# Kernel optimization log

Measured on AMD Instinct MI355X. Metric: run time of the kernel, lower is better.

## Reference

```python
import jax, jax.numpy as jnp
import numpy as np

HIDDEN = 1024
NHEAD = 16
HEAD_DIM = HIDDEN // NHEAD
B, S = 2, 2048


def setup_inputs() -> dict:
    key = jax.random.key(0)
    ks = jax.random.split(key, 10)
    scale = 1.0 / np.sqrt(HIDDEN)
    inp = {
        "x": jax.random.normal(ks[0], (B, S, HIDDEN), dtype=jnp.float32),
        "mask": jax.random.randint(ks[1], (B, S), 0, 2).astype(bool),
        "Wq": jax.random.normal(ks[2], (HIDDEN, HIDDEN), dtype=jnp.float32) * scale,
        "bq": jnp.zeros((HIDDEN,), dtype=jnp.float32),
        "Wk": jax.random.normal(ks[3], (HIDDEN, HIDDEN), dtype=jnp.float32) * scale,
        "bk": jnp.zeros((HIDDEN,), dtype=jnp.float32),
        "Wv": jax.random.normal(ks[4], (HIDDEN, HIDDEN), dtype=jnp.float32) * scale,
        "bv": jnp.zeros((HIDDEN,), dtype=jnp.float32),
        "Wo": jax.random.normal(ks[5], (HIDDEN, HIDDEN), dtype=jnp.float32) * scale,
        "bo": jnp.zeros((HIDDEN,), dtype=jnp.float32),
    }
    return inp


def reference(x, mask, Wq, bq, Wk, bk, Wv, bv, Wo, bo):
    B_, S_, H = x.shape
    # QKV projections (torch Linear: x @ W.T + b), split into heads -> [B, nhead, S, head_dim]
    def split_heads(t):
        return t.reshape(B_, S_, NHEAD, HEAD_DIM).transpose(0, 2, 1, 3)

    q = split_heads(x @ Wq.T + bq)
    k = split_heads(x @ Wk.T + bk)
    v = split_heads(x @ Wv.T + bv)

    # scaled dot-product scores: [B, nhead, S, S]
    energy = jnp.einsum("bhqd,bhkd->bhqk", q, k) / jnp.sqrt(jnp.float32(HEAD_DIM))

    # combined padding + diagonal-exclusion mask: mask keys where mask[b,k] is True,
    # but never mask the diagonal (self) position
    eye = jnp.eye(S_, dtype=bool)  # [S, S]
    attn_mask = mask[:, None, None, :] & ~eye[None, None, :, :]  # [B, 1, S, S] broadcast over heads
    energy = jnp.where(attn_mask, -jnp.inf, energy)

    attention = jax.nn.softmax(energy, axis=-1)
    out = jnp.einsum("bhqk,bhkd->bhqd", attention, v)  # [B, nhead, S, head_dim]
    out = out.transpose(0, 2, 1, 3).reshape(B_, S_, H)
    return out @ Wo.T + bo
```

## Files before the change

### kernel.cpp

```cpp
#include <hip/hip_runtime.h>

typedef __attribute__((ext_vector_type(8))) short short8;
typedef __attribute__((ext_vector_type(4))) float f32x4;
typedef __attribute__((ext_vector_type(16))) float f32x16;
typedef __attribute__((ext_vector_type(4))) unsigned short ushort4v;

#define HIDDEN 1024
#define NHEAD 16
#define HD 64
#define BATCH 2
#define SEQ 2048
#define MROWS (BATCH * SEQ)
#define QSCALE 0.18033688011112042f

__device__ __forceinline__ unsigned short f2b(float f) {
  union { float f; unsigned u; } v; v.f = f;
  unsigned r = v.u + 0x7fffu + ((v.u >> 16) & 1u);
  return (unsigned short)(r >> 16);
}

__device__ __forceinline__ unsigned cvt_pk_bf16(float lo, float hi) {
  unsigned r;
  asm("v_cvt_pk_bf16_f32 %0, %1, %2" : "=v"(r) : "v"(lo), "v"(hi));
  return r;
}

__device__ __forceinline__ float fexp2(float x) {
#if __has_builtin(__builtin_amdgcn_exp2f)
  return __builtin_amdgcn_exp2f(x);
#else
  return exp2f(x);
#endif
}

__device__ __forceinline__ void gll16(const void* g, void* l) {
  __builtin_amdgcn_global_load_lds(
      (__attribute__((address_space(1))) void*)g,
      (__attribute__((address_space(3))) void*)l, 16, 0, 0);
}

__global__ void prep_kernel(const float* __restrict__ x,
                            const float* __restrict__ Wq,
                            const float* __restrict__ Wk,
                            const float* __restrict__ Wv,
                            const float* __restrict__ Wo,
                            unsigned short* __restrict__ xb,
                            unsigned short* __restrict__ wqb,
                            unsigned short* __restrict__ wkb,
                            unsigned short* __restrict__ wvb,
                            unsigned short* __restrict__ wob) {
  int bid = blockIdx.x;
  const float* src;
  unsigned short* dst;
  int base;
  if (bid < 4096)      { src = x;  dst = xb;  base = bid; }
  else if (bid < 5120) { src = Wq; dst = wqb; base = bid - 4096; }
  else if (bid < 6144) { src = Wk; dst = wkb; base = bid - 5120; }
  else if (bid < 7168) { src = Wv; dst = wvb; base = bid - 6144; }
  else                 { src = Wo; dst = wob; base = bid - 7168; }
  int i = (base * 256 + threadIdx.x) * 4;
  float4 v = *reinterpret_cast<const float4*>(src + i);
  ushort4v o;
  o.x = f2b(v.x); o.y = f2b(v.y); o.z = f2b(v.z); o.w = f2b(v.w);
  *reinterpret_cast<ushort4v*>(dst + i) = o;
}

__global__ void amask_kernel(const int* __restrict__ m, float* __restrict__ am,
                             int n) {
  int i = blockIdx.x * blockDim.x + threadIdx.x;
  if (i < n) am[i] = m[i] ? -1e30f : 0.f;
}

template <int MODE>
__global__ __launch_bounds__(256) void gemm128_kernel(
    const unsigned short* __restrict__ A,
    const unsigned short* __restrict__ W0,
    const unsigned short* __restrict__ W1,
    const unsigned short* __restrict__ W2,
    const float* __restrict__ c0, const float* __restrict__ c1,
    const float* __restrict__ c2, void* __restrict__ o0,
    void* __restrict__ o1, void* __restrict__ o2) {
  __shared__ __align__(16) unsigned short Al[2][128 * 64];
  __shared__ __align__(16) unsigned short Bl[2][128 * 64];
  const int t = threadIdx.x;
  const int w = t >> 6, l = t & 63;
  const int hi = l >> 4, lo16 = l & 15;
  const int wr = w >> 1, wc = w & 1;
  const int F = blockIdx.y * gridDim.x + blockIdx.x;
  const int chunk = (gridDim.x * gridDim.y) >> 3;
  const int L = (F & 7) * chunk + (F >> 3);
  const int m0 = (L % gridDim.x) * 128;
  const int n0 = (L / gridDim.x) * 128;
  const int K = HIDDEN;

  const unsigned short* Bsel;
  const float* bias;
  int region = 0, n_loc = n0;
  if (MODE == 0) {
    region = n0 >> 10;
    n_loc = n0 & 1023;
    Bsel = region == 0 ? W0 : (region == 1 ? W1 : W2);
    bias = region == 0 ? c0 : (region == 1 ? c1 : c2);
  } else {
    Bsel = W0;
    bias = c0;
  }

  const int srow = w * 32 + (l >> 3);
  const int schunk = (l & 7) ^ (l >> 3);
  const int rsw = (lo16 & 7);

  const unsigned short* pA[4];
  const unsigned short* pB[4];
#pragma unroll
  for (int i = 0; i < 4; ++i) {
    pA[i] = A + (size_t)(m0 + srow + i * 8) * K + schunk * 8;
    pB[i] = Bsel + (size_t)(n_loc + srow + i * 8) * K + schunk * 8;
  }

  f32x4 acc[4][4];
#pragma unroll
  for (int mi = 0; mi < 4; ++mi)
#pragma unroll
    for (int f = 0; f < 4; ++f) acc[mi][f] = f32x4{0.f, 0.f, 0.f, 0.f};

#pragma unroll
  for (int i = 0; i < 4; ++i) {
    gll16(pA[i], &Al[0][(w * 32 + i * 8) * 64]);
    gll16(pB[i], &Bl[0][(w * 32 + i * 8) * 64]);
    pA[i] += 64; pB[i] += 64;
  }
  __syncthreads();

  auto step = [&](int knext, int BUF) __attribute__((always_inline)) {
    if (knext < K) {
#pragma unroll
      for (int i = 0; i < 4; ++i) {
        gll16(pA[i], &Al[BUF ^ 1][(w * 32 + i * 8) * 64]);
        gll16(pB[i], &Bl[BUF ^ 1][(w * 32 + i * 8) * 64]);
        pA[i] += 64; pB[i] += 64;
      }
    }
#pragma unroll
    for (int kk = 0; kk < 2; ++kk) {
      short8 af[4], bf[4];
#pragma unroll
      for (int mi = 0; mi < 4; ++mi) {
        int row = wr * 64 + mi * 16 + lo16;
        af[mi] = *reinterpret_cast<const short8*>(
            &Al[BUF][row * 64 + (((kk * 4 + hi) ^ rsw) * 8)]);
      }
#pragma unroll
      for (int f = 0; f < 4; ++f) {
        int row = wc * 64 + f * 16 + lo16;
        bf[f] = *reinterpret_cast<const short8*>(
            &Bl[BUF][row * 64 + (((kk * 4 + hi) ^ rsw) * 8)]);
      }
#pragma unroll
      for (int mi = 0; mi < 4; ++mi)
#pragma unroll
        for (int f = 0; f < 4; ++f)
          acc[mi][f] =
              __builtin_amdgcn_mfma_f32_16x16x32_bf16(af[mi], bf[f], acc[mi][f], 0, 0, 0);
    }
    __syncthreads();
  };

  for (int kt = 0; kt < K; kt += 128) {
    step(kt + 64, 0);
    step(kt + 128, 1);
  }

#pragma unroll
  for (int mi = 0; mi < 4; ++mi)
#pragma unroll
    for (int f = 0; f < 4; ++f) {
      int mbase = m0 + wr * 64 + mi * 16 + hi * 4;
      int n_rel = n_loc + wc * 64 + f * 16 + lo16;
      float bv_ = bias[n_rel];
      if (MODE == 0 && region == 2) {
        int b = mbase >> 11, s = mbase & 2047, d = n_rel & 63, h = n_rel >> 6;
        uint2 pk;
        pk.x = cvt_pk_bf16(acc[mi][f][0] + bv_, acc[mi][f][1] + bv_);
        pk.y = cvt_pk_bf16(acc[mi][f][2] + bv_, acc[mi][f][3] + bv_);
        *reinterpret_cast<uint2*>(
            (unsigned short*)o2 + ((size_t)(b * NHEAD + h) * HD + d) * SEQ + s) = pk;
        continue;
      }
#pragma unroll
      for (int j = 0; j < 4; ++j) {
        float v = acc[mi][f][j] + bv_;
        int mm = mbase + j;
        if (MODE == 0) {
          int b = mm >> 11, s = mm & 2047, h = n_rel >> 6, d = n_rel & 63;
          if (region == 0)
            ((unsigned short*)o0)[((size_t)(b * NHEAD + h) * SEQ + s) * HD + d] =
                f2b(v * QSCALE);
          else
            ((unsigned short*)o1)[((size_t)(b * NHEAD + h) * SEQ + s) * HD + d] =
                f2b(v);
        } else {
          ((float*)o0)[(size_t)mm * HIDDEN + n_rel] = v;
        }
      }
    }
}

__global__ __launch_bounds__(512) void attn_kernel(
    const unsigned short* __restrict__ Q, const unsigned short* __restrict__ Km,
    const unsigned short* __restrict__ Vt, const float* __restrict__ amf,
    unsigned short* __restrict__ O) {
  __shared__ __align__(16) unsigned short KV[3][2][64 * 64];
  __shared__ float SrwS[4][64];
  const int t = threadIdx.x;
  const int w = t >> 6, l = t & 63;
  const int q31 = l & 31, hi32 = l >> 5;
  const int qg = w >> 1, half = w & 1;
  const int nb = ((blockIdx.x & 7) << 6) | (blockIdx.x >> 3);
  const int qt = nb & 15, bh = nb >> 4;
  const int b = bh >> 4, h = bh & 15;
  const int q0w = qt * 128 + qg * 32;
  const int q = q0w + q31;
  const bool diagw = (half == (qg & 1));
  const int dtile = qt * 128 + (qg >> 1) * 64;

  const unsigned short* Qb = Q + (size_t)bh * SEQ * HD;
  const unsigned short* Kb = Km + (size_t)bh * SEQ * HD;
  const unsigned short* Vb = Vt + (size_t)bh * HD * SEQ;
  const float* mb = amf + b * SEQ + half * 32;

  short8 qf[4];
#pragma unroll
  for (int dc = 0; dc < 4; ++dc)
    qf[dc] = *reinterpret_cast<const short8*>(
        Qb + (size_t)q * HD + dc * 16 + hi32 * 8);

  f32x16 o0, o1;
#pragma unroll
  for (int r = 0; r < 16; ++r) { o0[r] = 0.f; o1[r] = 0.f; }
  float srw = 0.f;

  const int srow = w * 8 + (l >> 3);
  const int sc_ = ((l & 7) ^ (l >> 3) ^ (w & 3)) * 8;
  const unsigned short* pK = Kb + (size_t)srow * HD + sc_;
  const unsigned short* pV = Vb + (size_t)srow * SEQ + sc_;

  gll16(pK, &KV[0][0][(w * 8) * 64]);
  gll16(pV, &KV[0][1][(w * 8) * 64]);
  pK += 64 * HD; pV += 64;
  gll16(pK, &KV[1][0][(w * 8) * 64]);
  gll16(pV, &KV[1][1][(w * 8) * 64]);
  pK += 64 * HD; pV += 64;
  asm volatile("s_waitcnt vmcnt(2)" ::: "memory");
  __builtin_amdgcn_s_barrier();
  __builtin_amdgcn_sched_barrier(0);

  const int rk = (q31 & 7) ^ (q31 >> 3);

  auto step = [&](int k0, int BUF, int NBUF) __attribute__((always_inline)) {
    float4 a0[4];
#pragma unroll
    for (int g = 0; g < 4; ++g)
      a0[g] = *reinterpret_cast<const float4*>(mb + k0 + g * 8 + hi32 * 4);

    if (k0 + 128 < SEQ) {
      gll16(pK, &KV[NBUF][0][(w * 8) * 64]);
      gll16(pV, &KV[NBUF][1][(w * 8) * 64]);
      pK += 64 * HD; pV += 64;
    }

    f32x16 s0;
    if (diagw && k0 == dtile) {
      int kb = hi32 * 4;
#pragma unroll
      for (int g = 0; g < 4; ++g) {
        if (kb + g * 8 + 0 == q31) a0[g].x = 0.f;
        if (kb + g * 8 + 1 == q31) a0[g].y = 0.f;
        if (kb + g * 8 + 2 == q31) a0[g].z = 0.f;
        if (kb + g * 8 + 3 == q31) a0[g].w = 0.f;
      }
    }
#pragma unroll
    for (int g = 0; g < 4; ++g) {
      s0[4 * g + 0] = a0[g].x; s0[4 * g + 1] = a0[g].y;
      s0[4 * g + 2] = a0[g].z; s0[4 * g + 3] = a0[g].w;
    }

    __builtin_amdgcn_s_setprio(1);
#pragma unroll
    for (int dc = 0; dc < 4; ++dc) {
      short8 kf = *reinterpret_cast<const short8*>(
          &KV[BUF][0][(half * 32 + q31) * 64 + (((dc * 2 + hi32) ^ rk) * 8)]);
      s0 = __builtin_amdgcn_mfma_f32_32x32x16_bf16(kf, qf[dc], s0, 0, 0, 0);
    }
    __builtin_amdgcn_s_setprio(0);

    float sum = 0.f;
#pragma unroll
    for (int r = 0; r < 16; ++r) {
      float p = fexp2(s0[r]);
      s0[r] = p;
      sum += p;
    }
    {
      unsigned a = __float_as_uint(sum), bsw = a;
      auto rr = __builtin_amdgcn_permlane32_swap(a, bsw, false, false);
      sum = __uint_as_float(rr[0]) + __uint_as_float(rr[1]);
    }
    srw += sum;

    unsigned c[8];
#pragma unroll
    for (int R = 0; R < 4; ++R) {
      c[R * 2 + 0] = cvt_pk_bf16(s0[4 * R + 0], s0[4 * R + 1]);
      c[R * 2 + 1] = cvt_pk_bf16(s0[4 * R + 2], s0[4 * R + 3]);
    }

    short8 pb[2];
#pragma unroll
    for (int sl = 0; sl < 2; ++sl) {
      const int R0 = sl * 2;
      auto r0 = __builtin_amdgcn_permlane32_swap(c[R0 * 2 + 0],
                                                 c[(R0 + 1) * 2 + 0], false, false);
      auto r1 = __builtin_amdgcn_permlane32_swap(c[R0 * 2 + 1],
                                                 c[(R0 + 1) * 2 + 1], false, false);
      union { unsigned u[4]; short8 s8; } pu;
      pu.u[0] = r0[0]; pu.u[1] = r1[0]; pu.u[2] = r0[1]; pu.u[3] = r1[1];
      pb[sl] = pu.s8;
    }

    __builtin_amdgcn_s_setprio(1);
#pragma unroll
    for (int sl = 0; sl < 2; ++sl) {
      int ch = (((half * 2 + sl) * 2 + hi32) ^ rk) * 8;
      short8 vf0 = *reinterpret_cast<const short8*>(&KV[BUF][1][q31 * 64 + ch]);
      short8 vf1 =
          *reinterpret_cast<const short8*>(&KV[BUF][1][(32 + q31) * 64 + ch]);
      o0 = __builtin_amdgcn_mfma_f32_32x32x16_bf16(vf0, pb[sl], o0, 0, 0, 0);
      o1 = __builtin_amdgcn_mfma_f32_32x32x16_bf16(vf1, pb[sl], o1, 0, 0, 0);
    }
    __builtin_amdgcn_s_setprio(0);

    asm volatile("s_waitcnt vmcnt(2)" ::: "memory");
    __builtin_amdgcn_s_barrier();
    __builtin_amdgcn_sched_barrier(0);
  };

  for (int tt = 0; tt < 30; tt += 3) {
    step(tt * 64, 0, 2);
    step((tt + 1) * 64, 1, 0);
    step((tt + 2) * 64, 2, 1);
  }
  step(30 * 64, 0, 2);
  step(31 * 64, 1, 0);

  float* obuf = (float*)&KV[0][0][0];
  if (half) {
    float* d = obuf + (qg * 64 + l) * 33;
#pragma unroll
    for (int r = 0; r < 16; ++r) { d[r] = o0[r]; d[16 + r] = o1[r]; }
    SrwS[qg][l] = srw;
  }
  __syncthreads();
  if (!half) {
    const float* d = obuf + (qg * 64 + l) * 33;
#pragma unroll
    for (int r = 0; r < 16; ++r) { o0[r] += d[r]; o1[r] += d[16 + r]; }
    srw += SrwS[qg][l];

    float rinv = 1.f / srw;
    unsigned short* Ob = O + (size_t)(b * SEQ + q) * HIDDEN + h * HD;
#pragma unroll
    for (int g = 0; g < 4; ++g) {
      uint2 w0, w1;
      w0.x = cvt_pk_bf16(o0[4 * g + 0] * rinv, o0[4 * g + 1] * rinv);
      w0.y = cvt_pk_bf16(o0[4 * g + 2] * rinv, o0[4 * g + 3] * rinv);
      w1.x = cvt_pk_bf16(o1[4 * g + 0] * rinv, o1[4 * g + 1] * rinv);
      w1.y = cvt_pk_bf16(o1[4 * g + 2] * rinv, o1[4 * g + 3] * rinv);
      *reinterpret_cast<uint2*>(Ob + 8 * g + 4 * hi32) = w0;
      *reinterpret_cast<uint2*>(Ob + 32 + 8 * g + 4 * hi32) = w1;
    }
  }
}

extern "C" void kernel_launch(void* const* d_in, const int* in_sizes, int n_in,
                              void* d_out, int out_size, void* d_ws,
                              size_t ws_size, hipStream_t stream) {
  const float* x = (const float*)d_in[0];
  const int* mask = (const int*)d_in[1];
  const float* Wq = (const float*)d_in[2];
  const float* bq = (const float*)d_in[3];
  const float* Wk = (const float*)d_in[4];
  const float* bk = (const float*)d_in[5];
  const float* Wv = (const float*)d_in[6];
  const float* bv = (const float*)d_in[7];
  const float* Wo = (const float*)d_in[8];
  const float* bo = (const float*)d_in[9];

  char* ws = (char*)d_ws;
  unsigned short* xb  = (unsigned short*)(ws + ((size_t)0 << 20));
  unsigned short* wqb = (unsigned short*)(ws + ((size_t)8 << 20));
  unsigned short* wkb = (unsigned short*)(ws + ((size_t)10 << 20));
  unsigned short* wvb = (unsigned short*)(ws + ((size_t)12 << 20));
  unsigned short* wob = (unsigned short*)(ws + ((size_t)14 << 20));
  unsigned short* qw  = (unsigned short*)(ws + ((size_t)16 << 20));
  unsigned short* kw  = (unsigned short*)(ws + ((size_t)24 << 20));
  unsigned short* vtw = (unsigned short*)(ws + ((size_t)32 << 20));
  unsigned short* ow  = (unsigned short*)(ws + ((size_t)40 << 20));
  float* amf = (float*)(ws + ((size_t)0 << 20));

  prep_kernel<<<8192, 256, 0, stream>>>(x, Wq, Wk, Wv, Wo, xb, wqb, wkb, wvb,
                                        wob);

  gemm128_kernel<0><<<dim3(MROWS / 128, 3 * HIDDEN / 128), 256, 0, stream>>>(
      xb, wqb, wkb, wvb, bq, bk, bv, qw, kw, vtw);

  amask_kernel<<<MROWS / 256, 256, 0, stream>>>(mask, amf, MROWS);

  attn_kernel<<<512, 512, 0, stream>>>(qw, kw, vtw, amf, ow);

  gemm128_kernel<1><<<dim3(MROWS / 128, HIDDEN / 128), 256, 0, stream>>>(
      ow, wob, nullptr, nullptr, bo, nullptr, nullptr, d_out, nullptr, nullptr);
}
```

Before: 133.1 us.

## Switch GEMM to triple-buffered 32-wide K tiles with counted vmcnt waits

After: 137.7 us. 1.03x slower.

```diff
diff --git a/kernel.cpp b/kernel.cpp
--- a/kernel.cpp
+++ b/kernel.cpp
@@ -80,17 +80,14 @@
     const float* __restrict__ c0, const float* __restrict__ c1,
     const float* __restrict__ c2, void* __restrict__ o0,
     void* __restrict__ o1, void* __restrict__ o2) {
-  __shared__ __align__(16) unsigned short Al[2][128 * 64];
-  __shared__ __align__(16) unsigned short Bl[2][128 * 64];
+  __shared__ __align__(16) unsigned short Al[3][128 * 32];
+  __shared__ __align__(16) unsigned short Bl[3][128 * 32];
   const int t = threadIdx.x;
   const int w = t >> 6, l = t & 63;
   const int hi = l >> 4, lo16 = l & 15;
   const int wr = w >> 1, wc = w & 1;
-  const int F = blockIdx.y * gridDim.x + blockIdx.x;
-  const int chunk = (gridDim.x * gridDim.y) >> 3;
-  const int L = (F & 7) * chunk + (F >> 3);
-  const int m0 = (L % gridDim.x) * 128;
-  const int n0 = (L / gridDim.x) * 128;
+  const int m0 = blockIdx.x * 128;
+  const int n0 = blockIdx.y * 128;
   const int K = HIDDEN;
 
   const unsigned short* Bsel;
@@ -106,16 +103,14 @@
     bias = c0;
   }
 
-  const int srow = w * 32 + (l >> 3);
-  const int schunk = (l & 7) ^ (l >> 3);
-  const int rsw = (lo16 & 7);
-
-  const unsigned short* pA[4];
-  const unsigned short* pB[4];
-#pragma unroll
-  for (int i = 0; i < 4; ++i) {
-    pA[i] = A + (size_t)(m0 + srow + i * 8) * K + schunk * 8;
-    pB[i] = Bsel + (size_t)(n_loc + srow + i * 8) * K + schunk * 8;
+  const int srow0 = w * 16 + (l >> 2);
+  const int schunk = ((l & 3) ^ ((l >> 2) & 3)) * 8;
+  const unsigned short* pA[2];
+  const unsigned short* pB[2];
+#pragma unroll
+  for (int i = 0; i < 2; ++i) {
+    pA[i] = A + (size_t)(m0 + i * 64 + srow0) * K + schunk;
+    pB[i] = Bsel + (size_t)(n_loc + i * 64 + srow0) * K + schunk;
   }
 
   f32x4 acc[4][4];
@@ -124,52 +119,58 @@
 #pragma unroll
     for (int f = 0; f < 4; ++f) acc[mi][f] = f32x4{0.f, 0.f, 0.f, 0.f};
 
-#pragma unroll
-  for (int i = 0; i < 4; ++i) {
-    gll16(pA[i], &Al[0][(w * 32 + i * 8) * 64]);
-    gll16(pB[i], &Bl[0][(w * 32 + i * 8) * 64]);
-    pA[i] += 64; pB[i] += 64;
-  }
-  __syncthreads();
-
-  auto step = [&](int knext, int BUF) __attribute__((always_inline)) {
-    if (knext < K) {
-#pragma unroll
-      for (int i = 0; i < 4; ++i) {
-        gll16(pA[i], &Al[BUF ^ 1][(w * 32 + i * 8) * 64]);
-        gll16(pB[i], &Bl[BUF ^ 1][(w * 32 + i * 8) * 64]);
-        pA[i] += 64; pB[i] += 64;
-      }
-    }
-#pragma unroll
-    for (int kk = 0; kk < 2; ++kk) {
-      short8 af[4], bf[4];
-#pragma unroll
-      for (int mi = 0; mi < 4; ++mi) {
-        int row = wr * 64 + mi * 16 + lo16;
-        af[mi] = *reinterpret_cast<const short8*>(
-            &Al[BUF][row * 64 + (((kk * 4 + hi) ^ rsw) * 8)]);
-      }
-#pragma unroll
-      for (int f = 0; f < 4; ++f) {
-        int row = wc * 64 + f * 16 + lo16;
-        bf[f] = *reinterpret_cast<const short8*>(
-            &Bl[BUF][row * 64 + (((kk * 4 + hi) ^ rsw) * 8)]);
-      }
-#pragma unroll
-      for (int mi = 0; mi < 4; ++mi)
-#pragma unroll
-        for (int f = 0; f < 4; ++f)
-          acc[mi][f] =
-              __builtin_amdgcn_mfma_f32_16x16x32_bf16(af[mi], bf[f], acc[mi][f], 0, 0, 0);
-    }
-    __syncthreads();
+  auto stage = [&](int BUF) __attribute__((always_inline)) {
+#pragma unroll
+    for (int i = 0; i < 2; ++i) {
+      gll16(pA[i], &Al[BUF][(i * 64 + w * 16) * 32]);
+      gll16(pB[i], &Bl[BUF][(i * 64 + w * 16) * 32]);
+      pA[i] += 32; pB[i] += 32;
+    }
   };
 
-  for (int kt = 0; kt < K; kt += 128) {
-    step(kt + 64, 0);
-    step(kt + 128, 1);
-  }
+  stage(0);
+  stage(1);
+  asm volatile("s_waitcnt vmcnt(4)" ::: "memory");
+  __builtin_amdgcn_s_barrier();
+  __builtin_amdgcn_sched_barrier(0);
+
+  const int rsl = lo16 & 3;
+
+  auto step = [&](int tt, int BUF, int NBUF, int WAITN) __attribute__((always_inline)) {
+    if (tt + 2 < 32) stage(NBUF);
+    short8 af[4], bf[4];
+#pragma unroll
+    for (int mi = 0; mi < 4; ++mi)
+      af[mi] = *reinterpret_cast<const short8*>(
+          &Al[BUF][(wr * 64 + mi * 16 + lo16) * 32 + ((hi ^ rsl) * 8)]);
+#pragma unroll
+    for (int f = 0; f < 4; ++f)
+      bf[f] = *reinterpret_cast<const short8*>(
+          &Bl[BUF][(wc * 64 + f * 16 + lo16) * 32 + ((hi ^ rsl) * 8)]);
+#pragma unroll
+    for (int mi = 0; mi < 4; ++mi)
+#pragma unroll
+      for (int f = 0; f < 4; ++f)
+        acc[mi][f] =
+            __builtin_amdgcn_mfma_f32_16x16x32_bf16(af[mi], bf[f], acc[mi][f], 0, 0, 0);
+    if (WAITN >= 0) {
+      if (WAITN == 4)
+        asm volatile("s_waitcnt vmcnt(4)" ::: "memory");
+      else
+        asm volatile("s_waitcnt vmcnt(0)" ::: "memory");
+      __builtin_amdgcn_s_barrier();
+      __builtin_amdgcn_sched_barrier(0);
+    }
+  };
+
+#pragma unroll 1
+  for (int g = 0; g < 30; g += 3) {
+    step(g + 0, 0, 2, 4);
+    step(g + 1, 1, 0, 4);
+    step(g + 2, 2, 1, 4);
+  }
+  step(30, 0, 2, 0);
+  step(31, 1, 0, -1);
 
 #pragma unroll
   for (int mi = 0; mi < 4; ++mi)
@@ -257,7 +258,7 @@
 
   const int rk = (q31 & 7) ^ (q31 >> 3);
 
-  auto step = [&](int k0, int BUF, int NBUF) __attribute__((always_inline)) {
+  auto step = [&](int k0, int BUF, int NBUF, int WAITN) __attribute__((always_inline)) {
     float4 a0[4];
 #pragma unroll
     for (int g = 0; g < 4; ++g)
@@ -341,18 +342,21 @@
     }
     __builtin_amdgcn_s_setprio(0);
 
-    asm volatile("s_waitcnt vmcnt(2)" ::: "memory");
+    if (WAITN == 2)
+      asm volatile("s_waitcnt vmcnt(2)" ::: "memory");
+    else
+      asm volatile("s_waitcnt vmcnt(0)" ::: "memory");
     __builtin_amdgcn_s_barrier();
     __builtin_amdgcn_sched_barrier(0);
   };
 
   for (int tt = 0; tt < 30; tt += 3) {
-    step(tt * 64, 0, 2);
-    step((tt + 1) * 64, 1, 0);
-    step((tt + 2) * 64, 2, 1);
-  }
-  step(30 * 64, 0, 2);
-  step(31 * 64, 1, 0);
+    step(tt * 64, 0, 2, 2);
+    step((tt + 1) * 64, 1, 0, 2);
+    step((tt + 2) * 64, 2, 1, 2);
+  }
+  step(30 * 64, 0, 2, 0);
+  step(31 * 64, 1, 0, 0);
 
   float* obuf = (float*)&KV[0][0][0];
   if (half) {
```

## Split output projection into dedicated 64x128-tile GEMM and drop block swizzle

Applied to the files above, without the earlier changes.

New measurement: 121.9 us. 8.4% less time.

```diff
diff --git a/kernel.cpp b/kernel.cpp
--- a/kernel.cpp
+++ b/kernel.cpp
@@ -71,8 +71,7 @@
   if (i < n) am[i] = m[i] ? -1e30f : 0.f;
 }
 
-template <int MODE>
-__global__ __launch_bounds__(256) void gemm128_kernel(
+__global__ __launch_bounds__(256) void gemm_qkv_kernel(
     const unsigned short* __restrict__ A,
     const unsigned short* __restrict__ W0,
     const unsigned short* __restrict__ W1,
@@ -86,25 +85,14 @@
   const int w = t >> 6, l = t & 63;
   const int hi = l >> 4, lo16 = l & 15;
   const int wr = w >> 1, wc = w & 1;
-  const int F = blockIdx.y * gridDim.x + blockIdx.x;
-  const int chunk = (gridDim.x * gridDim.y) >> 3;
-  const int L = (F & 7) * chunk + (F >> 3);
-  const int m0 = (L % gridDim.x) * 128;
-  const int n0 = (L / gridDim.x) * 128;
+  const int m0 = blockIdx.x * 128;
+  const int n0 = blockIdx.y * 128;
   const int K = HIDDEN;
 
-  const unsigned short* Bsel;
-  const float* bias;
-  int region = 0, n_loc = n0;
-  if (MODE == 0) {
-    region = n0 >> 10;
-    n_loc = n0 & 1023;
-    Bsel = region == 0 ? W0 : (region == 1 ? W1 : W2);
-    bias = region == 0 ? c0 : (region == 1 ? c1 : c2);
-  } else {
-    Bsel = W0;
-    bias = c0;
-  }
+  const int region = n0 >> 10;
+  const int n_loc = n0 & 1023;
+  const unsigned short* Bsel = region == 0 ? W0 : (region == 1 ? W1 : W2);
+  const float* bias = region == 0 ? c0 : (region == 1 ? c1 : c2);
 
   const int srow = w * 32 + (l >> 3);
   const int schunk = (l & 7) ^ (l >> 3);
@@ -178,7 +166,7 @@
       int mbase = m0 + wr * 64 + mi * 16 + hi * 4;
       int n_rel = n_loc + wc * 64 + f * 16 + lo16;
       float bv_ = bias[n_rel];
-      if (MODE == 0 && region == 2) {
+      if (region == 2) {
         int b = mbase >> 11, s = mbase & 2047, d = n_rel & 63, h = n_rel >> 6;
         uint2 pk;
         pk.x = cvt_pk_bf16(acc[mi][f][0] + bv_, acc[mi][f][1] + bv_);
@@ -191,18 +179,101 @@
       for (int j = 0; j < 4; ++j) {
         float v = acc[mi][f][j] + bv_;
         int mm = mbase + j;
-        if (MODE == 0) {
-          int b = mm >> 11, s = mm & 2047, h = n_rel >> 6, d = n_rel & 63;
-          if (region == 0)
-            ((unsigned short*)o0)[((size_t)(b * NHEAD + h) * SEQ + s) * HD + d] =
-                f2b(v * QSCALE);
-          else
-            ((unsigned short*)o1)[((size_t)(b * NHEAD + h) * SEQ + s) * HD + d] =
-                f2b(v);
-        } else {
-          ((float*)o0)[(size_t)mm * HIDDEN + n_rel] = v;
-        }
-      }
+        int b = mm >> 11, s = mm & 2047, h = n_rel >> 6, d = n_rel & 63;
+        if (region == 0)
+          ((unsigned short*)o0)[((size_t)(b * NHEAD + h) * SEQ + s) * HD + d] =
+              f2b(v * QSCALE);
+        else
+          ((unsigned short*)o1)[((size_t)(b * NHEAD + h) * SEQ + s) * HD + d] =
+              f2b(v);
+      }
+    }
+}
+
+__global__ __launch_bounds__(256) void gemm_o_kernel(
+    const unsigned short* __restrict__ A, const unsigned short* __restrict__ W0,
+    const float* __restrict__ bias, float* __restrict__ out) {
+  __shared__ __align__(16) unsigned short Al[2][64 * 64];
+  __shared__ __align__(16) unsigned short Bl[2][128 * 64];
+  const int t = threadIdx.x;
+  const int w = t >> 6, l = t & 63;
+  const int hi = l >> 4, lo16 = l & 15;
+  const int m0 = blockIdx.x * 64;
+  const int n0 = blockIdx.y * 128;
+  const int K = HIDDEN;
+
+  const int schunk = (l & 7) ^ (l >> 3);
+  const int rsw = (lo16 & 7);
+
+  const unsigned short* pA[2];
+#pragma unroll
+  for (int i = 0; i < 2; ++i)
+    pA[i] = A + (size_t)(m0 + w * 16 + i * 8 + (l >> 3)) * K + schunk * 8;
+  const unsigned short* pB[4];
+#pragma unroll
+  for (int i = 0; i < 4; ++i)
+    pB[i] = W0 + (size_t)(n0 + w * 32 + i * 8 + (l >> 3)) * K + schunk * 8;
+
+  f32x4 acc[4][2];
+#pragma unroll
+  for (int mi = 0; mi < 4; ++mi)
+#pragma unroll
+    for (int f = 0; f < 2; ++f) acc[mi][f] = f32x4{0.f, 0.f, 0.f, 0.f};
+
+  auto stage = [&](int BUF) __attribute__((always_inline)) {
+#pragma unroll
+    for (int i = 0; i < 2; ++i) {
+      gll16(pA[i], &Al[BUF][(w * 16 + i * 8) * 64]);
+      pA[i] += 64;
+    }
+#pragma unroll
+    for (int i = 0; i < 4; ++i) {
+      gll16(pB[i], &Bl[BUF][(w * 32 + i * 8) * 64]);
+      pB[i] += 64;
+    }
+  };
+
+  stage(0);
+  __syncthreads();
+
+  auto step = [&](int knext, int BUF) __attribute__((always_inline)) {
+    if (knext < K) stage(BUF ^ 1);
+#pragma unroll
+    for (int kk = 0; kk < 2; ++kk) {
+      short8 af[4], bf[2];
+#pragma unroll
+      for (int mi = 0; mi < 4; ++mi)
+        af[mi] = *reinterpret_cast<const short8*>(
+            &Al[BUF][(mi * 16 + lo16) * 64 + (((kk * 4 + hi) ^ rsw) * 8)]);
+#pragma unroll
+      for (int f = 0; f < 2; ++f)
+        bf[f] = *reinterpret_cast<const short8*>(
+            &Bl[BUF][(w * 32 + f * 16 + lo16) * 64 + (((kk * 4 + hi) ^ rsw) * 8)]);
+#pragma unroll
+      for (int mi = 0; mi < 4; ++mi)
+#pragma unroll
+        for (int f = 0; f < 2; ++f)
+          acc[mi][f] =
+              __builtin_amdgcn_mfma_f32_16x16x32_bf16(af[mi], bf[f], acc[mi][f], 0, 0, 0);
+    }
+    __syncthreads();
+  };
+
+  for (int kt = 0; kt < K; kt += 128) {
+    step(kt + 64, 0);
+    step(kt + 128, 1);
+  }
+
+#pragma unroll
+  for (int mi = 0; mi < 4; ++mi)
+#pragma unroll
+    for (int f = 0; f < 2; ++f) {
+      int mbase = m0 + mi * 16 + hi * 4;
+      int n = n0 + w * 32 + f * 16 + lo16;
+      float bv_ = bias[n];
+#pragma unroll
+      for (int j = 0; j < 4; ++j)
+        out[(size_t)(mbase + j) * HIDDEN + n] = acc[mi][f][j] + bv_;
     }
 }
 
@@ -257,7 +328,7 @@
 
   const int rk = (q31 & 7) ^ (q31 >> 3);
 
-  auto step = [&](int k0, int BUF, int NBUF) __attribute__((always_inline)) {
+  auto step = [&](int k0, int BUF, int NBUF, int WAITN) __attribute__((always_inline)) {
     float4 a0[4];
 #pragma unroll
     for (int g = 0; g < 4; ++g)
@@ -341,18 +412,21 @@
     }
     __builtin_amdgcn_s_setprio(0);
 
-    asm volatile("s_waitcnt vmcnt(2)" ::: "memory");
+    if (WAITN == 2)
+      asm volatile("s_waitcnt vmcnt(2)" ::: "memory");
+    else
+      asm volatile("s_waitcnt vmcnt(0)" ::: "memory");
     __builtin_amdgcn_s_barrier();
     __builtin_amdgcn_sched_barrier(0);
   };
 
   for (int tt = 0; tt < 30; tt += 3) {
-    step(tt * 64, 0, 2);
-    step((tt + 1) * 64, 1, 0);
-    step((tt + 2) * 64, 2, 1);
-  }
-  step(30 * 64, 0, 2);
-  step(31 * 64, 1, 0);
+    step(tt * 64, 0, 2, 2);
+    step((tt + 1) * 64, 1, 0, 2);
+    step((tt + 2) * 64, 2, 1, 2);
+  }
+  step(30 * 64, 0, 2, 0);
+  step(31 * 64, 1, 0, 0);
 
   float* obuf = (float*)&KV[0][0][0];
   if (half) {
@@ -412,13 +486,13 @@
   prep_kernel<<<8192, 256, 0, stream>>>(x, Wq, Wk, Wv, Wo, xb, wqb, wkb, wvb,
                                         wob);
 
-  gemm128_kernel<0><<<dim3(MROWS / 128, 3 * HIDDEN / 128), 256, 0, stream>>>(
+  gemm_qkv_kernel<<<dim3(MROWS / 128, 3 * HIDDEN / 128), 256, 0, stream>>>(
       xb, wqb, wkb, wvb, bq, bk, bv, qw, kw, vtw);
 
   amask_kernel<<<MROWS / 256, 256, 0, stream>>>(mask, amf, MROWS);
 
   attn_kernel<<<512, 512, 0, stream>>>(qw, kw, vtw, amf, ow);
 
-  gemm128_kernel<1><<<dim3(MROWS / 128, HIDDEN / 128), 256, 0, stream>>>(
-      ow, wob, nullptr, nullptr, bo, nullptr, nullptr, d_out, nullptr, nullptr);
-}
+  gemm_o_kernel<<<dim3(MROWS / 64, HIDDEN / 128), 256, 0, stream>>>(
+      ow, wob, bo, (float*)d_out);
+}
```
